# Optimization experiments

Measured on AMD Instinct MI355X. Metric: run time of the kernel, lower is better.

The kernel has to match this reference:

```python
import jax, jax.numpy as jnp
import numpy as np

EMB_SIZE = 768
BLOCK_SIZE = 64
OFFSET = 1  # bert cls offset


def setup_inputs() -> dict:
    key = jax.random.key(0)
    ks = jax.random.split(key, 10)
    n, c, d, h, E, M, P = 4, 1024, 768, 12, 42, 8, 1024
    sequence_output = jax.random.normal(ks[0], (n, c, d), jnp.float32)
    attention = jax.random.uniform(ks[1], (n, h, c, c), jnp.float32)
    attention = attention / attention.sum(-1, keepdims=True)  # softmax-like rows
    Wh = jax.random.normal(ks[2], (EMB_SIZE, 2 * d), jnp.float32) * 0.02
    bh = jax.random.normal(ks[3], (EMB_SIZE,), jnp.float32) * 0.02
    Wt = jax.random.normal(ks[4], (EMB_SIZE, 2 * d), jnp.float32) * 0.02
    bt = jax.random.normal(ks[5], (EMB_SIZE,), jnp.float32) * 0.02
    Wb = jax.random.normal(ks[6], (99, EMB_SIZE * BLOCK_SIZE), jnp.float32) * 0.02
    mention_pos = jax.random.randint(ks[7], (n, E, M), 0, c - 1 - OFFSET, jnp.int32)
    mention_mask = jax.random.randint(ks[8], (n, E, M), 0, 2, jnp.int32)
    mention_mask = mention_mask.at[:, :, 0].set(1)  # every entity has >=1 mention
    hts = jax.random.randint(ks[9], (n, P, 2), 0, E, jnp.int32)
    return {"sequence_output": sequence_output, "attention": attention,
            "Wh": Wh, "bh": bh, "Wt": Wt, "bt": bt, "Wb": Wb,
            "mention_pos": mention_pos, "mention_mask": mention_mask, "hts": hts}


def _get_hrt_doc(seq, att, pos, mask, ht):
    # seq [c,d], att [h,c,c], pos/mask [E,M], ht [P,2]
    p = pos + OFFSET                                   # [E,M]
    valid = mask > 0
    memb = seq[p]                                      # [E,M,d] gather
    e_emb = jax.scipy.special.logsumexp(
        jnp.where(valid[..., None], memb, -jnp.inf), axis=1)  # [E,d]
    matt = att[:, p]                                   # [h,E,M,c] gather
    cnt = valid.sum(1).astype(seq.dtype)               # [E]
    e_att = (matt * valid[None, :, :, None].astype(seq.dtype)).sum(2)
    e_att = jnp.transpose(e_att, (1, 0, 2)) / cnt[:, None, None]  # [E,h,c] mention mean
    hs = e_emb[ht[:, 0]]                               # [P,d]
    ts = e_emb[ht[:, 1]]
    h_att = e_att[ht[:, 0]]                            # [P,h,c]
    t_att = e_att[ht[:, 1]]
    ht_att = (h_att * t_att).mean(1)                   # [P,c] head mean
    ht_att = ht_att / (ht_att.sum(1, keepdims=True) + 1e-5)
    rs = jnp.einsum('ld,rl->rd', seq, ht_att)          # [P,d]
    return hs, ts, rs


def reference(sequence_output, attention, Wh, bh, Wt, bt, Wb,
              mention_pos, mention_mask, hts):
    d = sequence_output.shape[-1]
    hs, ts, rs = jax.vmap(_get_hrt_doc)(sequence_output, attention,
                                        mention_pos, mention_mask, hts)
    hs = hs.reshape(-1, d)
    ts = ts.reshape(-1, d)
    rs = rs.reshape(-1, d)
    hs = jnp.tanh(jnp.concatenate([hs, rs], axis=1) @ Wh.T + bh)
    ts = jnp.tanh(jnp.concatenate([ts, rs], axis=1) @ Wt.T + bt)
    nb = EMB_SIZE // BLOCK_SIZE
    b1 = hs.reshape(-1, nb, BLOCK_SIZE)
    b2 = ts.reshape(-1, nb, BLOCK_SIZE)
    bl = (b1[:, :, :, None] * b2[:, :, None, :]).reshape(-1, EMB_SIZE * BLOCK_SIZE)
    logits = bl @ Wb.T                                 # [N, num_labels+2]
    return logits
```

## Files before the change

### kernel.cpp

```cpp
#include <hip/hip_runtime.h>
#include <hip/hip_bf16.h>
#include <hip/hip_fp16.h>
#include <math.h>

#define NDOC 4
#define CCC  1024
#define DDD  768
#define HHH  12
#define EEE  42
#define MMM  8
#define PPP  1024
#define NBQ  12
#define NK   99
#define NPAD 112

typedef __attribute__((ext_vector_type(8))) short short8v;
typedef __attribute__((ext_vector_type(8))) _Float16 half8;
typedef __attribute__((ext_vector_type(4))) float floatx4;

__device__ __forceinline__ unsigned short f32_to_bf16u(float f) {
  return __builtin_bit_cast(unsigned short, __float2bfloat16(f));
}
__device__ __forceinline__ unsigned short f32_to_f16u(float f) {
  return __builtin_bit_cast(unsigned short, __float2half(f));
}

__global__ __launch_bounds__(256) void k_eemb(const float* __restrict__ seq,
    const int* __restrict__ pos, const int* __restrict__ mask,
    unsigned short* __restrict__ eembB) {
  int e = blockIdx.x, doc = blockIdx.y;
  int base = (doc*EEE + e)*MMM;
  int p[MMM], mk[MMM];
#pragma unroll
  for (int m = 0; m < MMM; ++m) { p[m] = pos[base+m] + 1; mk[m] = mask[base+m]; }
  for (int d0 = threadIdx.x; d0 < DDD; d0 += 256) {
    float v[MMM]; float mx = -INFINITY;
#pragma unroll
    for (int m = 0; m < MMM; ++m) {
      v[m] = seq[(doc*CCC + p[m])*DDD + d0];
      if (mk[m]) mx = fmaxf(mx, v[m]);
    }
    float s = 0.f;
#pragma unroll
    for (int m = 0; m < MMM; ++m) if (mk[m]) s += expf(v[m]-mx);
    eembB[(doc*EEE + e)*DDD + d0] = f32_to_bf16u(logf(s) + mx);
  }
}

__global__ __launch_bounds__(256) void k_eatt(const float* __restrict__ att,
    const int* __restrict__ pos, const int* __restrict__ mask,
    float* __restrict__ eatt) {
  int head = blockIdx.x, e = blockIdx.y, doc = blockIdx.z;
  int base = (doc*EEE + e)*MMM;
  int j = threadIdx.x * 4;
  float ax=0.f, ay=0.f, az=0.f, aw=0.f; float cnt = 0.f;
#pragma unroll
  for (int m = 0; m < MMM; ++m) {
    int mk = mask[base+m];
    cnt += (float)mk;
    if (mk) {
      int pp = pos[base+m] + 1;
      const float4 a = *(const float4*)&att[((size_t)(doc*HHH + head)*CCC + pp)*CCC + j];
      ax += a.x; ay += a.y; az += a.z; aw += a.w;
    }
  }
  float inv = 1.f / cnt;
  float4 o; o.x = ax*inv; o.y = ay*inv; o.z = az*inv; o.w = aw*inv;
  *(float4*)&eatt[((size_t)((doc*EEE + e)*HHH + head))*CCC + j] = o;
}

__global__ __launch_bounds__(256) void k_htatt(const float* __restrict__ eatt,
    const int* __restrict__ hts, unsigned short* __restrict__ htB) {
  int b = blockIdx.x; int doc = b >> 10; int r = b & 1023;
  int h0 = hts[(doc*PPP + r)*2 + 0];
  int t0 = hts[(doc*PPP + r)*2 + 1];
  const float* ea0 = &eatt[(size_t)((doc*EEE + h0)*HHH)*CCC];
  const float* ea1 = &eatt[(size_t)((doc*EEE + t0)*HHH)*CCC];
  int j = threadIdx.x * 4;
  float vx=0.f, vy=0.f, vz=0.f, vw=0.f;
#pragma unroll
  for (int hh = 0; hh < HHH; ++hh) {
    const float4 a  = *(const float4*)&ea0[hh*CCC + j];
    const float4 bq = *(const float4*)&ea1[hh*CCC + j];
    vx += a.x*bq.x; vy += a.y*bq.y; vz += a.z*bq.z; vw += a.w*bq.w;
  }
  const float inv12 = 1.f/12.f;
  vx *= inv12; vy *= inv12; vz *= inv12; vw *= inv12;
  float part = vx + vy + vz + vw;
  __shared__ float red[4];
  for (int off = 32; off > 0; off >>= 1) part += __shfl_down(part, off, 64);
  int lane = threadIdx.x & 63, wv = threadIdx.x >> 6;
  if (lane == 0) red[wv] = part;
  __syncthreads();
  if (threadIdx.x == 0) red[0] = red[0]+red[1]+red[2]+red[3];
  __syncthreads();
  float sc = 1.f / (red[0] + 1e-5f);
  unsigned short o[4];
  o[0] = f32_to_bf16u(vx*sc); o[1] = f32_to_bf16u(vy*sc);
  o[2] = f32_to_bf16u(vz*sc); o[3] = f32_to_bf16u(vw*sc);
  *(uint2*)&htB[((size_t)(doc*PPP + r))*CCC + j] = *(const uint2*)o;
}

__global__ __launch_bounds__(256) void k_packW(const float* __restrict__ Wh,
    const float* __restrict__ Wt, unsigned short* __restrict__ WB) {
  int gid = blockIdx.x*256 + threadIdx.x;
  int half = gid >= 147456;
  int loc = half ? gid - 147456 : gid;
  const float* src = (half ? Wt : Wh) + (size_t)loc*8;
  float4 v0 = *(const float4*)src;
  float4 v1 = *(const float4*)(src+4);
  unsigned short o[8];
  o[0]=f32_to_bf16u(v0.x); o[1]=f32_to_bf16u(v0.y); o[2]=f32_to_bf16u(v0.z); o[3]=f32_to_bf16u(v0.w);
  o[4]=f32_to_bf16u(v1.x); o[5]=f32_to_bf16u(v1.y); o[6]=f32_to_bf16u(v1.z); o[7]=f32_to_bf16u(v1.w);
  *(uint4*)&WB[(size_t)half*1179648 + (size_t)loc*8] = *(const uint4*)o;
}

__global__ __launch_bounds__(256) void k_seqT(const float* __restrict__ seq,
    unsigned short* __restrict__ seqTB) {
  __shared__ float tl[64][65];
  int d0 = blockIdx.x * 64, c0 = blockIdx.y * 64, doc = blockIdx.z;
  int t = threadIdx.x;
#pragma unroll
  for (int rep = 0; rep < 4; ++rep) {
    int cr = rep*16 + (t >> 4);
    int d4 = (t & 15) * 4;
    float4 v = *(const float4*)&seq[((size_t)doc*CCC + c0 + cr)*DDD + d0 + d4];
    tl[cr][d4+0]=v.x; tl[cr][d4+1]=v.y; tl[cr][d4+2]=v.z; tl[cr][d4+3]=v.w;
  }
  __syncthreads();
#pragma unroll
  for (int rep = 0; rep < 4; ++rep) {
    int dr = rep*16 + (t >> 4);
    int c4 = (t & 15) * 4;
    unsigned short o[4];
#pragma unroll
    for (int kq = 0; kq < 4; ++kq)
      o[kq] = f32_to_bf16u(tl[c4+kq][dr]);
    *(uint2*)&seqTB[((size_t)doc*DDD + d0 + dr)*CCC + c0 + c4] = *(const uint2*)o;
  }
}

__global__ __launch_bounds__(256) void k_rs_mfma(
    const unsigned short* __restrict__ htB,
    const unsigned short* __restrict__ seqTB,
    unsigned short* __restrict__ rsB) {
  __shared__ unsigned short A_l[4096];
  __shared__ unsigned short B_l[4096];
  const int n0 = blockIdx.x * 128;
  const int m0 = blockIdx.y * 128;
  const int doc = m0 >> 10;
  const int mloc = m0 & 1023;
  const int t = threadIdx.x;
  const int lane = t & 63;
  const int ln = lane & 15, q4 = lane >> 4;
  const int w = t >> 6;
  const int wr = w >> 1, wc = w & 1;

  const int r0 = t >> 2;
  const int koff = (t & 3) * 8;
  const unsigned short* srcA0 = htB + ((size_t)doc*CCC + mloc + r0)*CCC + koff;
  const unsigned short* srcA1 = htB + ((size_t)doc*CCC + mloc + r0 + 64)*CCC + koff;
  const unsigned short* srcB0 = seqTB + ((size_t)doc*DDD + n0 + r0)*CCC + koff;
  const unsigned short* srcB1 = seqTB + ((size_t)doc*DDD + n0 + r0 + 64)*CCC + koff;

  floatx4 acc[4][4];
#pragma unroll
  for (int i = 0; i < 4; ++i)
#pragma unroll
    for (int j = 0; j < 4; ++j) acc[i][j] = (floatx4){0.f,0.f,0.f,0.f};

  for (int k0 = 0; k0 < CCC; k0 += 32) {
    uint4 va0 = *(const uint4*)(srcA0 + k0);
    uint4 va1 = *(const uint4*)(srcA1 + k0);
    uint4 vb0 = *(const uint4*)(srcB0 + k0);
    uint4 vb1 = *(const uint4*)(srcB1 + k0);
    __syncthreads();
    *(uint4*)&A_l[(size_t)t*8]       = va0;
    *(uint4*)&A_l[(size_t)(t+256)*8] = va1;
    *(uint4*)&B_l[(size_t)t*8]       = vb0;
    *(uint4*)&B_l[(size_t)(t+256)*8] = vb1;
    __syncthreads();
    short8v a[4], b[4];
#pragma unroll
    for (int rt = 0; rt < 4; ++rt)
      a[rt] = *(const short8v*)&A_l[((wr*64 + rt*16 + ln)*4 + q4)*8];
#pragma unroll
    for (int nt = 0; nt < 4; ++nt)
      b[nt] = *(const short8v*)&B_l[((wc*64 + nt*16 + ln)*4 + q4)*8];
#pragma unroll
    for (int rt = 0; rt < 4; ++rt)
#pragma unroll
      for (int nt = 0; nt < 4; ++nt)
        acc[rt][nt] = __builtin_amdgcn_mfma_f32_16x16x32_bf16(a[rt], b[nt], acc[rt][nt], 0, 0, 0);
  }
#pragma unroll
  for (int rt = 0; rt < 4; ++rt)
#pragma unroll
    for (int nt = 0; nt < 4; ++nt) {
      int col = n0 + wc*64 + nt*16 + ln;
#pragma unroll
      for (int reg = 0; reg < 4; ++reg) {
        int row = m0 + wr*64 + rt*16 + q4*4 + reg;
        rsB[(size_t)row*DDD + col] = f32_to_bf16u(acc[rt][nt][reg]);
      }
    }
}

__global__ __launch_bounds__(256) void k_heads_mfma(
    const unsigned short* __restrict__ eembB,
    const unsigned short* __restrict__ rsB,
    const int* __restrict__ hts,
    const unsigned short* __restrict__ WB,
    const float* __restrict__ bh, const float* __restrict__ bt,
    float* __restrict__ hsb, float* __restrict__ tsb) {
  __shared__ unsigned short A_l[4096];
  __shared__ unsigned short B_l[4096];
  const int which = blockIdx.z;
  const int n0 = blockIdx.x * 128;
  const int m0 = blockIdx.y * 128;
  const int doc = m0 >> 10;
  const int t = threadIdx.x;
  const int lane = t & 63;
  const int ln = lane & 15, q4 = lane >> 4;
  const int w = t >> 6;
  const int wr = w >> 1, wc = w & 1;

  const int r0 = t >> 2;
  const int koff = (t & 3) * 8;
  const int rgA0 = m0 + r0, rgA1 = m0 + r0 + 64;
  const int idx0 = hts[rgA0*2 + which];
  const int idx1 = hts[rgA1*2 + which];
  const unsigned short* srcE0 = eembB + (size_t)(doc*EEE + idx0)*DDD + koff;
  const unsigned short* srcE1 = eembB + (size_t)(doc*EEE + idx1)*DDD + koff;
  const unsigned short* srcR0 = rsB + (size_t)rgA0*DDD + koff;
  const unsigned short* srcR1 = rsB + (size_t)rgA1*DDD + koff;
  const unsigned short* WBz = WB + (size_t)which*1179648;
  const unsigned short* srcW0 = WBz + (size_t)(n0 + r0)*1536 + koff;
  const unsigned short* srcW1 = WBz + (size_t)(n0 + r0 + 64)*1536 + koff;

  floatx4 acc[4][4];
#pragma unroll
  for (int i = 0; i < 4; ++i)
#pragma unroll
    for (int j = 0; j < 4; ++j) acc[i][j] = (floatx4){0.f,0.f,0.f,0.f};

  for (int k0 = 0; k0 < 1536; k0 += 32) {
    uint4 va0 = (k0 < DDD) ? *(const uint4*)(srcE0 + k0) : *(const uint4*)(srcR0 + (k0 - DDD));
    uint4 va1 = (k0 < DDD) ? *(const uint4*)(srcE1 + k0) : *(const uint4*)(srcR1 + (k0 - DDD));
    uint4 vb0 = *(const uint4*)(srcW0 + k0);
    uint4 vb1 = *(const uint4*)(srcW1 + k0);
    __syncthreads();
    *(uint4*)&A_l[(size_t)t*8]       = va0;
    *(uint4*)&A_l[(size_t)(t+256)*8] = va1;
    *(uint4*)&B_l[(size_t)t*8]       = vb0;
    *(uint4*)&B_l[(size_t)(t+256)*8] = vb1;
    __syncthreads();
    short8v a[4], b[4];
#pragma unroll
    for (int rt = 0; rt < 4; ++rt)
      a[rt] = *(const short8v*)&A_l[((wr*64 + rt*16 + ln)*4 + q4)*8];
#pragma unroll
    for (int nt = 0; nt < 4; ++nt)
      b[nt] = *(const short8v*)&B_l[((wc*64 + nt*16 + ln)*4 + q4)*8];
#pragma unroll
    for (int rt = 0; rt < 4; ++rt)
#pragma unroll
      for (int nt = 0; nt < 4; ++nt)
        acc[rt][nt] = __builtin_amdgcn_mfma_f32_16x16x32_bf16(a[rt], b[nt], acc[rt][nt], 0, 0, 0);
  }
  const float* bias = which ? bt : bh;
  float* outp = which ? tsb : hsb;
#pragma unroll
  for (int rt = 0; rt < 4; ++rt)
#pragma unroll
    for (int nt = 0; nt < 4; ++nt) {
      int col = n0 + wc*64 + nt*16 + ln;
      float bsv = bias[col];
#pragma unroll
      for (int reg = 0; reg < 4; ++reg) {
        int row = m0 + wr*64 + rt*16 + q4*4 + reg;
        outp[(size_t)row*DDD + col] = tanhf(acc[rt][nt][reg] + bsv);
      }
    }
}

__global__ __launch_bounds__(256) void k_prep_w(const float* __restrict__ Wb,
    unsigned short* __restrict__ Wp) {
  int t = blockIdx.x*256 + threadIdx.x;
  int j8 = (t & 7) * 8;
  int n = (t >> 3) % NPAD;
  int ki = t / 896;
  unsigned short o[8];
  if (n < NK) {
    const float* src = &Wb[(size_t)n*49152 + ki*64 + j8];
    float4 v0 = *(const float4*)src;
    float4 v1 = *(const float4*)(src+4);
    o[0]=f32_to_f16u(v0.x); o[1]=f32_to_f16u(v0.y); o[2]=f32_to_f16u(v0.z); o[3]=f32_to_f16u(v0.w);
    o[4]=f32_to_f16u(v1.x); o[5]=f32_to_f16u(v1.y); o[6]=f32_to_f16u(v1.z); o[7]=f32_to_f16u(v1.w);
  } else {
#pragma unroll
    for (int e=0;e<8;++e) o[e]=0;
  }
  int js = (t & 7) >> 2, q = t & 3;
  int nt = n >> 4, lnn = n & 15;
  int c = ((js*7 + nt)*4 + q)*16 + lnn;
  *(uint4*)&Wp[(size_t)ki*7168 + c*8] = *(const uint4*)o;
}

__global__ __launch_bounds__(256) void k_pack_hs(const float* __restrict__ hs,
    unsigned short* __restrict__ hsT) {
  __shared__ float tl[64][65];
  int i0 = blockIdx.x * 64, r0 = blockIdx.y * 64;
  int t = threadIdx.x;
#pragma unroll
  for (int rep = 0; rep < 4; ++rep) {
    int r = rep*16 + (t >> 4);
    int c4 = (t & 15) * 4;
    float4 v = *(const float4*)&hs[(size_t)(r0 + r)*DDD + i0 + c4];
    tl[r][c4+0]=v.x; tl[r][c4+1]=v.y; tl[r][c4+2]=v.z; tl[r][c4+3]=v.w;
  }
  __syncthreads();
#pragma unroll
  for (int rep = 0; rep < 4; ++rep) {
    int i = rep*16 + (t >> 4);
    int r4 = (t & 15) * 4;
    unsigned short o[4];
#pragma unroll
    for (int kq = 0; kq < 4; ++kq)
      o[kq] = f32_to_f16u(tl[r4+kq][i]);
    *(uint2*)&hsT[(size_t)(i0 + i)*4096 + r0 + r4] = *(const uint2*)o;
  }
}

__global__ __launch_bounds__(128, 2) void k_logits_mfma(
    const unsigned short* __restrict__ hsT,
    const float* __restrict__ tsb,
    const unsigned short* __restrict__ Wp,
    unsigned short* __restrict__ P) {
  __shared__ unsigned short hsT_l[32*128];
  __shared__ unsigned short Bt_l[2*7168];
  const int slice = blockIdx.x;
  const int kbase = (slice >> 1)*64 + (slice & 1)*32;
  const int mtile = blockIdx.y;
  const int t = threadIdx.x;
  const int w = t >> 6;
  const int lane = t & 63;
  const int ln = lane & 15;
  const int q = lane >> 4;
  const int m0w = mtile*128 + w*64;

#pragma unroll
  for (int rep = 0; rep < 4; ++rep) {
    int c16 = t + rep*128;
    int ii = c16 >> 4;
    int c8 = (c16 & 15) * 8;
    uint4 v = *(const uint4*)&hsT[(size_t)(kbase + ii)*4096 + mtile*128 + c8];
    *(uint4*)&hsT_l[ii*128 + c8] = v;
  }

  __half2 tsr2[4][2][4];
  {
    int nb = kbase >> 6;
#pragma unroll
    for (int rt = 0; rt < 4; ++rt) {
      int row = m0w + rt*16 + ln;
#pragma unroll
      for (int js = 0; js < 2; ++js) {
        const float* p = &tsb[(size_t)row*DDD + nb*64 + js*32 + q*8];
        float4 v0 = *(const float4*)p;
        float4 v1 = *(const float4*)(p+4);
        tsr2[rt][js][0] = __floats2half2_rn(v0.x, v0.y);
        tsr2[rt][js][1] = __floats2half2_rn(v0.z, v0.w);
        tsr2[rt][js][2] = __floats2half2_rn(v1.x, v1.y);
        tsr2[rt][js][3] = __floats2half2_rn(v1.z, v1.w);
      }
    }
  }

  floatx4 acc[4][7];
#pragma unroll
  for (int rt = 0; rt < 4; ++rt)
#pragma unroll
    for (int nt = 0; nt < 7; ++nt)
      acc[rt][nt] = (floatx4){0.f,0.f,0.f,0.f};

  uint4 wreg[7];
#pragma unroll
  for (int r = 0; r < 7; ++r)
    wreg[r] = *(const uint4*)&Wp[(size_t)kbase*7168 + (t + r*128)*8];
#pragma unroll
  for (int r = 0; r < 7; ++r)
    *(uint4*)&Bt_l[(t + r*128)*8] = wreg[r];
  __syncthreads();

  for (int ii = 0; ii < 32; ++ii) {
    const unsigned short* bufc = Bt_l + (ii & 1)*7168;
    if (ii < 31) {
      int ki = kbase + ii + 1;
#pragma unroll
      for (int r = 0; r < 7; ++r)
        wreg[r] = *(const uint4*)&Wp[(size_t)ki*7168 + (t + r*128)*8];
    }
    __half2 hh[4];
#pragma unroll
    for (int rt = 0; rt < 4; ++rt) {
      unsigned short hb = hsT_l[ii*128 + w*64 + rt*16 + ln];
      hh[rt] = __half2half2(__ushort_as_half(hb));
    }
#pragma unroll
    for (int js = 0; js < 2; ++js) {
      half8 a[4];
#pragma unroll
      for (int rt = 0; rt < 4; ++rt) {
        uint4 au;
        au.x = __builtin_bit_cast(unsigned int, __hmul2(hh[rt], tsr2[rt][js][0]));
        au.y = __builtin_bit_cast(unsigned int, __hmul2(hh[rt], tsr2[rt][js][1]));
        au.z = __builtin_bit_cast(unsigned int, __hmul2(hh[rt], tsr2[rt][js][2]));
        au.w = __builtin_bit_cast(unsigned int, __hmul2(hh[rt], tsr2[rt][js][3]));
        a[rt] = __builtin_bit_cast(half8, au);
      }
#pragma unroll
      for (int nt = 0; nt < 7; ++nt) {
        half8 b = __builtin_bit_cast(half8,
            *(const short8v*)&bufc[((js*7 + nt)*4)*128 + lane*8]);
#pragma unroll
        for (int rt = 0; rt < 4; ++rt)
          acc[rt][nt] = __builtin_amdgcn_mfma_f32_16x16x32_f16(a[rt], b, acc[rt][nt], 0, 0, 0);
      }
    }
    if (ii < 31) {
      __syncthreads();
#pragma unroll
      for (int r = 0; r < 7; ++r)
        *(uint4*)&Bt_l[((ii+1) & 1)*7168 + (t + r*128)*8] = wreg[r];
      __syncthreads();
    }
  }

  unsigned short* Ps = P + (size_t)slice*(4096*NPAD);
#pragma unroll
  for (int nt = 0; nt < 7; ++nt) {
    int col = nt*16 + ln;
#pragma unroll
    for (int rt = 0; rt < 4; ++rt) {
#pragma unroll
      for (int reg = 0; reg < 4; ++reg) {
        int row = m0w + rt*16 + q*4 + reg;
        Ps[(size_t)row*NPAD + col] = f32_to_f16u(acc[rt][nt][reg]);
      }
    }
  }
}

__global__ __launch_bounds__(256) void k_logred(const unsigned short* __restrict__ P,
    float* __restrict__ out) {
  int idx = blockIdx.x*256 + threadIdx.x;
  int r = idx / NPAD;
  int c = idx % NPAD;
  if (c >= NK) return;
  float s = 0.f;
#pragma unroll
  for (int sl = 0; sl < 24; ++sl)
    s += __half2float(__ushort_as_half(P[(size_t)sl*(4096*NPAD) + idx]));
  out[(size_t)r*NK + c] = s;
}

extern "C" void kernel_launch(void* const* d_in, const int* in_sizes, int n_in,
                              void* d_out, int out_size, void* d_ws, size_t ws_size,
                              hipStream_t stream) {
  const float* seq  = (const float*)d_in[0];
  const float* att  = (const float*)d_in[1];
  const float* Wh   = (const float*)d_in[2];
  const float* bh   = (const float*)d_in[3];
  const float* Wt   = (const float*)d_in[4];
  const float* bt   = (const float*)d_in[5];
  const float* Wb   = (const float*)d_in[6];
  const int* pos    = (const int*)d_in[7];
  const int* mask   = (const int*)d_in[8];
  const int* hts    = (const int*)d_in[9];
  float* out = (float*)d_out;

  float* ws = (float*)d_ws;
  float*          eatt  = ws;
  unsigned short* htB   = (unsigned short*)(ws + 2064384);
  unsigned short* eembB = (unsigned short*)(ws + 4161536);
  unsigned short* seqTB = (unsigned short*)(ws + 4226048);
  unsigned short* WhtB  = (unsigned short*)(ws + 5798912);
  unsigned short* rsB   = (unsigned short*)(ws + 6978560);
  float*          hsb   = ws + 8551424;
  float*          tsb   = ws + 11697152;
  unsigned short* WpB   = (unsigned short*)eatt;
  unsigned short* hsTB  = (unsigned short*)seqTB;
  unsigned short* Pp    = (unsigned short*)(ws + 5798912);

  k_eemb<<<dim3(EEE, NDOC), 256, 0, stream>>>(seq, pos, mask, eembB);
  k_eatt<<<dim3(HHH, EEE, NDOC), 256, 0, stream>>>(att, pos, mask, eatt);
  k_htatt<<<dim3(NDOC*PPP), 256, 0, stream>>>(eatt, hts, htB);
  k_packW<<<dim3(1152), 256, 0, stream>>>(Wh, Wt, WhtB);
  k_seqT<<<dim3(DDD/64, CCC/64, NDOC), 256, 0, stream>>>(seq, seqTB);
  k_rs_mfma<<<dim3(6, 32), 256, 0, stream>>>(htB, seqTB, rsB);
  k_prep_w<<<dim3(2688), 256, 0, stream>>>(Wb, WpB);
  k_heads_mfma<<<dim3(6, 32, 2), 256, 0, stream>>>(eembB, rsB, hts, WhtB, bh, bt, hsb, tsb);
  k_pack_hs<<<dim3(DDD/64, 4096/64), 256, 0, stream>>>(hsb, hsTB);
  k_logits_mfma<<<dim3(24, 32), 128, 0, stream>>>(hsTB, tsb, WpB, Pp);
  k_logred<<<dim3(4096*NPAD/256), 256, 0, stream>>>(Pp, out);
}
```

Measured before the change: 221.8 us.

## Merge prep kernels, restructure ht-attention via LDS tiles, emit fp16 heads directly

Five independent preprocessing kernels (entity embedding, entity attention, Wh/Wt pack, seq transpose, Wb pack) become one block-dispatched kernel, cutting launch overhead and serialization. The per-pair ht-attention kernel is split into a tiled pass that caches per-entity attention in LDS and writes partial sums, followed by a normalization pass. The heads GEMM now writes fp16 transposed hs through LDS and fp16 ts directly, which removes the separate pack_hs kernel and the fp32 intermediates. Costs are a larger workspace, an extra 16 MB unnormalized fp32 buffer, and more LDS per heads block, which may reduce occupancy.

```diff
diff --git a/kernel.cpp b/kernel.cpp
--- a/kernel.cpp
+++ b/kernel.cpp
@@ -10,9 +10,9 @@
 #define EEE  42
 #define MMM  8
 #define PPP  1024
-#define NBQ  12
 #define NK   99
 #define NPAD 112
+#define NSLICE 24
 
 typedef __attribute__((ext_vector_type(8))) short short8v;
 typedef __attribute__((ext_vector_type(8))) _Float16 half8;
@@ -25,119 +25,163 @@
   return __builtin_bit_cast(unsigned short, __float2half(f));
 }
 
-__global__ __launch_bounds__(256) void k_eemb(const float* __restrict__ seq,
+__global__ __launch_bounds__(256) void k_prep(
+    const float* __restrict__ seq, const float* __restrict__ att,
+    const float* __restrict__ Wh, const float* __restrict__ Wt,
+    const float* __restrict__ Wb,
     const int* __restrict__ pos, const int* __restrict__ mask,
-    unsigned short* __restrict__ eembB) {
-  int e = blockIdx.x, doc = blockIdx.y;
-  int base = (doc*EEE + e)*MMM;
-  int p[MMM], mk[MMM];
-#pragma unroll
-  for (int m = 0; m < MMM; ++m) { p[m] = pos[base+m] + 1; mk[m] = mask[base+m]; }
-  for (int d0 = threadIdx.x; d0 < DDD; d0 += 256) {
-    float v[MMM]; float mx = -INFINITY;
+    unsigned short* __restrict__ eembB, float* __restrict__ eatt,
+    unsigned short* __restrict__ WhtB, unsigned short* __restrict__ seqTB,
+    unsigned short* __restrict__ WpB) {
+  const int bx = blockIdx.x;
+  const int tid = threadIdx.x;
+  if (bx < 168) {
+    int e = bx % EEE, doc = bx / EEE;
+    int base = (doc*EEE + e)*MMM;
+    int p[MMM], mk[MMM];
+#pragma unroll
+    for (int m = 0; m < MMM; ++m) { p[m] = pos[base+m] + 1; mk[m] = mask[base+m]; }
+    for (int d0 = tid; d0 < DDD; d0 += 256) {
+      float v[MMM]; float mx = -INFINITY;
+#pragma unroll
+      for (int m = 0; m < MMM; ++m) {
+        v[m] = seq[(doc*CCC + p[m])*DDD + d0];
+        if (mk[m]) mx = fmaxf(mx, v[m]);
+      }
+      float s = 0.f;
+#pragma unroll
+      for (int m = 0; m < MMM; ++m) if (mk[m]) s += expf(v[m]-mx);
+      eembB[(doc*EEE + e)*DDD + d0] = f32_to_bf16u(logf(s) + mx);
+    }
+  } else if (bx < 2184) {
+    int b = bx - 168;
+    int head = b % HHH, e = (b/HHH) % EEE, doc = b / (HHH*EEE);
+    int base = (doc*EEE + e)*MMM;
+    int j = tid * 4;
+    float ax=0.f, ay=0.f, az=0.f, aw=0.f; float cnt = 0.f;
 #pragma unroll
     for (int m = 0; m < MMM; ++m) {
-      v[m] = seq[(doc*CCC + p[m])*DDD + d0];
-      if (mk[m]) mx = fmaxf(mx, v[m]);
-    }
-    float s = 0.f;
-#pragma unroll
-    for (int m = 0; m < MMM; ++m) if (mk[m]) s += expf(v[m]-mx);
-    eembB[(doc*EEE + e)*DDD + d0] = f32_to_bf16u(logf(s) + mx);
-  }
-}
-
-__global__ __launch_bounds__(256) void k_eatt(const float* __restrict__ att,
-    const int* __restrict__ pos, const int* __restrict__ mask,
-    float* __restrict__ eatt) {
-  int head = blockIdx.x, e = blockIdx.y, doc = blockIdx.z;
-  int base = (doc*EEE + e)*MMM;
-  int j = threadIdx.x * 4;
-  float ax=0.f, ay=0.f, az=0.f, aw=0.f; float cnt = 0.f;
-#pragma unroll
-  for (int m = 0; m < MMM; ++m) {
-    int mk = mask[base+m];
-    cnt += (float)mk;
-    if (mk) {
-      int pp = pos[base+m] + 1;
-      const float4 a = *(const float4*)&att[((size_t)(doc*HHH + head)*CCC + pp)*CCC + j];
-      ax += a.x; ay += a.y; az += a.z; aw += a.w;
-    }
-  }
-  float inv = 1.f / cnt;
-  float4 o; o.x = ax*inv; o.y = ay*inv; o.z = az*inv; o.w = aw*inv;
-  *(float4*)&eatt[((size_t)((doc*EEE + e)*HHH + head))*CCC + j] = o;
-}
-
-__global__ __launch_bounds__(256) void k_htatt(const float* __restrict__ eatt,
-    const int* __restrict__ hts, unsigned short* __restrict__ htB) {
-  int b = blockIdx.x; int doc = b >> 10; int r = b & 1023;
-  int h0 = hts[(doc*PPP + r)*2 + 0];
-  int t0 = hts[(doc*PPP + r)*2 + 1];
-  const float* ea0 = &eatt[(size_t)((doc*EEE + h0)*HHH)*CCC];
-  const float* ea1 = &eatt[(size_t)((doc*EEE + t0)*HHH)*CCC];
-  int j = threadIdx.x * 4;
-  float vx=0.f, vy=0.f, vz=0.f, vw=0.f;
-#pragma unroll
-  for (int hh = 0; hh < HHH; ++hh) {
-    const float4 a  = *(const float4*)&ea0[hh*CCC + j];
-    const float4 bq = *(const float4*)&ea1[hh*CCC + j];
-    vx += a.x*bq.x; vy += a.y*bq.y; vz += a.z*bq.z; vw += a.w*bq.w;
-  }
-  const float inv12 = 1.f/12.f;
-  vx *= inv12; vy *= inv12; vz *= inv12; vw *= inv12;
-  float part = vx + vy + vz + vw;
-  __shared__ float red[4];
-  for (int off = 32; off > 0; off >>= 1) part += __shfl_down(part, off, 64);
-  int lane = threadIdx.x & 63, wv = threadIdx.x >> 6;
-  if (lane == 0) red[wv] = part;
+      int mk = mask[base+m];
+      cnt += (float)mk;
+      if (mk) {
+        int pp = pos[base+m] + 1;
+        const float4 a = *(const float4*)&att[((size_t)(doc*HHH + head)*CCC + pp)*CCC + j];
+        ax += a.x; ay += a.y; az += a.z; aw += a.w;
+      }
+    }
+    float inv = 1.f / cnt;
+    float4 o; o.x = ax*inv; o.y = ay*inv; o.z = az*inv; o.w = aw*inv;
+    *(float4*)&eatt[((size_t)((doc*EEE + e)*HHH + head))*CCC + j] = o;
+  } else if (bx < 3336) {
+    int gid = (bx - 2184)*256 + tid;
+    int half = gid >= 147456;
+    int loc = half ? gid - 147456 : gid;
+    const float* src = (half ? Wt : Wh) + (size_t)loc*8;
+    float4 v0 = *(const float4*)src;
+    float4 v1 = *(const float4*)(src+4);
+    unsigned short o[8];
+    o[0]=f32_to_bf16u(v0.x); o[1]=f32_to_bf16u(v0.y); o[2]=f32_to_bf16u(v0.z); o[3]=f32_to_bf16u(v0.w);
+    o[4]=f32_to_bf16u(v1.x); o[5]=f32_to_bf16u(v1.y); o[6]=f32_to_bf16u(v1.z); o[7]=f32_to_bf16u(v1.w);
+    *(uint4*)&WhtB[(size_t)half*1179648 + (size_t)loc*8] = *(const uint4*)o;
+  } else if (bx < 4104) {
+    __shared__ float tl[64][65];
+    int b = bx - 3336;
+    int d0 = (b % 12)*64, c0 = ((b/12) % 16)*64, doc = b / 192;
+#pragma unroll
+    for (int rep = 0; rep < 4; ++rep) {
+      int cr = rep*16 + (tid >> 4);
+      int d4 = (tid & 15) * 4;
+      float4 v = *(const float4*)&seq[((size_t)doc*CCC + c0 + cr)*DDD + d0 + d4];
+      tl[cr][d4+0]=v.x; tl[cr][d4+1]=v.y; tl[cr][d4+2]=v.z; tl[cr][d4+3]=v.w;
+    }
+    __syncthreads();
+#pragma unroll
+    for (int rep = 0; rep < 4; ++rep) {
+      int dr = rep*16 + (tid >> 4);
+      int c4 = (tid & 15) * 4;
+      unsigned short o[4];
+#pragma unroll
+      for (int kq = 0; kq < 4; ++kq)
+        o[kq] = f32_to_bf16u(tl[c4+kq][dr]);
+      *(uint2*)&seqTB[((size_t)doc*DDD + d0 + dr)*CCC + c0 + c4] = *(const uint2*)o;
+    }
+  } else {
+    int t = (bx - 4104)*256 + tid;
+    int j8 = (t & 7) * 8;
+    int n = (t >> 3) % NPAD;
+    int ki = t / 896;
+    unsigned short o[8];
+    if (n < NK) {
+      const float* src = &Wb[(size_t)n*49152 + ki*64 + j8];
+      float4 v0 = *(const float4*)src;
+      float4 v1 = *(const float4*)(src+4);
+      o[0]=f32_to_f16u(v0.x); o[1]=f32_to_f16u(v0.y); o[2]=f32_to_f16u(v0.z); o[3]=f32_to_f16u(v0.w);
+      o[4]=f32_to_f16u(v1.x); o[5]=f32_to_f16u(v1.y); o[6]=f32_to_f16u(v1.z); o[7]=f32_to_f16u(v1.w);
+    } else {
+#pragma unroll
+      for (int e=0;e<8;++e) o[e]=0;
+    }
+    int js = (t & 7) >> 2, q = t & 3;
+    int nt = n >> 4, lnn = n & 15;
+    int c = ((js*7 + nt)*4 + q)*16 + lnn;
+    *(uint4*)&WpB[(size_t)ki*7168 + c*8] = *(const uint4*)o;
+  }
+}
+
+__global__ __launch_bounds__(256) void k_htatt1(const float* __restrict__ eatt,
+    const int* __restrict__ hts, float* __restrict__ htU,
+    float* __restrict__ Ssum) {
+  __shared__ float tile[EEE*16*12];
+  const int cg = blockIdx.x, doc = blockIdx.y;
+  const int c0 = cg * 16;
+  for (int idx = threadIdx.x; idx < EEE*16*12; idx += 256) {
+    int e = idx / 192, rem = idx % 192, h = rem / 16, cc = rem % 16;
+    tile[(e*16 + cc)*12 + h] =
+        eatt[((size_t)((doc*EEE + e)*HHH + h))*CCC + c0 + cc];
+  }
   __syncthreads();
-  if (threadIdx.x == 0) red[0] = red[0]+red[1]+red[2]+red[3];
+  const int cc = threadIdx.x & 15;
+  const int pg = threadIdx.x >> 4;
+  for (int it = 0; it < 64; ++it) {
+    int p = pg + it*16;
+    int h0 = hts[(doc*PPP + p)*2 + 0];
+    int t0 = hts[(doc*PPP + p)*2 + 1];
+    const float* a = &tile[(h0*16 + cc)*12];
+    const float* b = &tile[(t0*16 + cc)*12];
+    float4 a0 = *(const float4*)a,     b0 = *(const float4*)b;
+    float4 a1 = *(const float4*)(a+4), b1 = *(const float4*)(b+4);
+    float4 a2 = *(const float4*)(a+8), b2 = *(const float4*)(b+8);
+    float s = a0.x*b0.x + a0.y*b0.y + a0.z*b0.z + a0.w*b0.w
+            + a1.x*b1.x + a1.y*b1.y + a1.z*b1.z + a1.w*b1.w
+            + a2.x*b2.x + a2.y*b2.y + a2.z*b2.z + a2.w*b2.w;
+    s *= (1.f/12.f);
+    htU[((size_t)(doc*PPP + p))*CCC + c0 + cc] = s;
+    float r = s;
+    r += __shfl_xor(r, 1, 16);
+    r += __shfl_xor(r, 2, 16);
+    r += __shfl_xor(r, 4, 16);
+    r += __shfl_xor(r, 8, 16);
+    if (cc == 0) Ssum[((size_t)(doc*PPP + p))*64 + cg] = r;
+  }
+}
+
+__global__ __launch_bounds__(256) void k_htnorm(const float* __restrict__ htU,
+    const float* __restrict__ Ssum, unsigned short* __restrict__ htB) {
+  __shared__ float sc_sh;
+  const int b = blockIdx.x;
+  const int lane = threadIdx.x;
+  if (lane < 64) {
+    float r = Ssum[(size_t)b*64 + lane];
+    for (int off = 32; off > 0; off >>= 1) r += __shfl_down(r, off, 64);
+    if (lane == 0) sc_sh = 1.f / (r + 1e-5f);
+  }
   __syncthreads();
-  float sc = 1.f / (red[0] + 1e-5f);
+  float sc = sc_sh;
+  float4 v = *(const float4*)&htU[(size_t)b*CCC + lane*4];
   unsigned short o[4];
-  o[0] = f32_to_bf16u(vx*sc); o[1] = f32_to_bf16u(vy*sc);
-  o[2] = f32_to_bf16u(vz*sc); o[3] = f32_to_bf16u(vw*sc);
-  *(uint2*)&htB[((size_t)(doc*PPP + r))*CCC + j] = *(const uint2*)o;
-}
-
-__global__ __launch_bounds__(256) void k_packW(const float* __restrict__ Wh,
-    const float* __restrict__ Wt, unsigned short* __restrict__ WB) {
-  int gid = blockIdx.x*256 + threadIdx.x;
-  int half = gid >= 147456;
-  int loc = half ? gid - 147456 : gid;
-  const float* src = (half ? Wt : Wh) + (size_t)loc*8;
-  float4 v0 = *(const float4*)src;
-  float4 v1 = *(const float4*)(src+4);
-  unsigned short o[8];
-  o[0]=f32_to_bf16u(v0.x); o[1]=f32_to_bf16u(v0.y); o[2]=f32_to_bf16u(v0.z); o[3]=f32_to_bf16u(v0.w);
-  o[4]=f32_to_bf16u(v1.x); o[5]=f32_to_bf16u(v1.y); o[6]=f32_to_bf16u(v1.z); o[7]=f32_to_bf16u(v1.w);
-  *(uint4*)&WB[(size_t)half*1179648 + (size_t)loc*8] = *(const uint4*)o;
-}
-
-__global__ __launch_bounds__(256) void k_seqT(const float* __restrict__ seq,
-    unsigned short* __restrict__ seqTB) {
-  __shared__ float tl[64][65];
-  int d0 = blockIdx.x * 64, c0 = blockIdx.y * 64, doc = blockIdx.z;
-  int t = threadIdx.x;
-#pragma unroll
-  for (int rep = 0; rep < 4; ++rep) {
-    int cr = rep*16 + (t >> 4);
-    int d4 = (t & 15) * 4;
-    float4 v = *(const float4*)&seq[((size_t)doc*CCC + c0 + cr)*DDD + d0 + d4];
-    tl[cr][d4+0]=v.x; tl[cr][d4+1]=v.y; tl[cr][d4+2]=v.z; tl[cr][d4+3]=v.w;
-  }
-  __syncthreads();
-#pragma unroll
-  for (int rep = 0; rep < 4; ++rep) {
-    int dr = rep*16 + (t >> 4);
-    int c4 = (t & 15) * 4;
-    unsigned short o[4];
-#pragma unroll
-    for (int kq = 0; kq < 4; ++kq)
-      o[kq] = f32_to_bf16u(tl[c4+kq][dr]);
-    *(uint2*)&seqTB[((size_t)doc*DDD + d0 + dr)*CCC + c0 + c4] = *(const uint2*)o;
-  }
+  o[0] = f32_to_bf16u(v.x*sc); o[1] = f32_to_bf16u(v.y*sc);
+  o[2] = f32_to_bf16u(v.z*sc); o[3] = f32_to_bf16u(v.w*sc);
+  *(uint2*)&htB[(size_t)b*CCC + lane*4] = *(const uint2*)o;
 }
 
 __global__ __launch_bounds__(256) void k_rs_mfma(
@@ -212,9 +256,11 @@
     const int* __restrict__ hts,
     const unsigned short* __restrict__ WB,
     const float* __restrict__ bh, const float* __restrict__ bt,
-    float* __restrict__ hsb, float* __restrict__ tsb) {
+    unsigned short* __restrict__ hsTB,
+    unsigned short* __restrict__ tsbH) {
   __shared__ unsigned short A_l[4096];
   __shared__ unsigned short B_l[4096];
+  __shared__ unsigned short T_l[128*144];
   const int which = blockIdx.z;
   const int n0 = blockIdx.x * 128;
   const int m0 = blockIdx.y * 128;
@@ -269,78 +315,53 @@
         acc[rt][nt] = __builtin_amdgcn_mfma_f32_16x16x32_bf16(a[rt], b[nt], acc[rt][nt], 0, 0, 0);
   }
   const float* bias = which ? bt : bh;
-  float* outp = which ? tsb : hsb;
-#pragma unroll
-  for (int rt = 0; rt < 4; ++rt)
-#pragma unroll
-    for (int nt = 0; nt < 4; ++nt) {
-      int col = n0 + wc*64 + nt*16 + ln;
-      float bsv = bias[col];
-#pragma unroll
-      for (int reg = 0; reg < 4; ++reg) {
-        int row = m0 + wr*64 + rt*16 + q4*4 + reg;
-        outp[(size_t)row*DDD + col] = tanhf(acc[rt][nt][reg] + bsv);
-      }
-    }
-}
-
-__global__ __launch_bounds__(256) void k_prep_w(const float* __restrict__ Wb,
-    unsigned short* __restrict__ Wp) {
-  int t = blockIdx.x*256 + threadIdx.x;
-  int j8 = (t & 7) * 8;
-  int n = (t >> 3) % NPAD;
-  int ki = t / 896;
-  unsigned short o[8];
-  if (n < NK) {
-    const float* src = &Wb[(size_t)n*49152 + ki*64 + j8];
-    float4 v0 = *(const float4*)src;
-    float4 v1 = *(const float4*)(src+4);
-    o[0]=f32_to_f16u(v0.x); o[1]=f32_to_f16u(v0.y); o[2]=f32_to_f16u(v0.z); o[3]=f32_to_f16u(v0.w);
-    o[4]=f32_to_f16u(v1.x); o[5]=f32_to_f16u(v1.y); o[6]=f32_to_f16u(v1.z); o[7]=f32_to_f16u(v1.w);
+  if (which == 0) {
+#pragma unroll
+    for (int rt = 0; rt < 4; ++rt)
+#pragma unroll
+      for (int nt = 0; nt < 4; ++nt) {
+        int col = wc*64 + nt*16 + ln;
+        float bsv = bias[n0 + col];
+#pragma unroll
+        for (int reg = 0; reg < 4; ++reg) {
+          int row = wr*64 + rt*16 + q4*4 + reg;
+          T_l[col*144 + row] = f32_to_f16u(tanhf(acc[rt][nt][reg] + bsv));
+        }
+      }
+    __syncthreads();
+#pragma unroll
+    for (int iter = 0; iter < 8; ++iter) {
+      int col = iter*16 + (t >> 4);
+      int rblk = t & 15;
+      uint4 v = *(const uint4*)&T_l[col*144 + rblk*8];
+      *(uint4*)&hsTB[(size_t)(n0 + col)*4096 + m0 + rblk*8] = v;
+    }
   } else {
 #pragma unroll
-    for (int e=0;e<8;++e) o[e]=0;
-  }
-  int js = (t & 7) >> 2, q = t & 3;
-  int nt = n >> 4, lnn = n & 15;
-  int c = ((js*7 + nt)*4 + q)*16 + lnn;
-  *(uint4*)&Wp[(size_t)ki*7168 + c*8] = *(const uint4*)o;
-}
-
-__global__ __launch_bounds__(256) void k_pack_hs(const float* __restrict__ hs,
-    unsigned short* __restrict__ hsT) {
-  __shared__ float tl[64][65];
-  int i0 = blockIdx.x * 64, r0 = blockIdx.y * 64;
-  int t = threadIdx.x;
-#pragma unroll
-  for (int rep = 0; rep < 4; ++rep) {
-    int r = rep*16 + (t >> 4);
-    int c4 = (t & 15) * 4;
-    float4 v = *(const float4*)&hs[(size_t)(r0 + r)*DDD + i0 + c4];
-    tl[r][c4+0]=v.x; tl[r][c4+1]=v.y; tl[r][c4+2]=v.z; tl[r][c4+3]=v.w;
-  }
-  __syncthreads();
-#pragma unroll
-  for (int rep = 0; rep < 4; ++rep) {
-    int i = rep*16 + (t >> 4);
-    int r4 = (t & 15) * 4;
-    unsigned short o[4];
-#pragma unroll
-    for (int kq = 0; kq < 4; ++kq)
-      o[kq] = f32_to_f16u(tl[r4+kq][i]);
-    *(uint2*)&hsT[(size_t)(i0 + i)*4096 + r0 + r4] = *(const uint2*)o;
-  }
-}
-
-__global__ __launch_bounds__(128, 2) void k_logits_mfma(
+    for (int rt = 0; rt < 4; ++rt)
+#pragma unroll
+      for (int nt = 0; nt < 4; ++nt) {
+        int col = n0 + wc*64 + nt*16 + ln;
+        float bsv = bias[col];
+#pragma unroll
+        for (int reg = 0; reg < 4; ++reg) {
+          int row = m0 + wr*64 + rt*16 + q4*4 + reg;
+          tsbH[(size_t)row*DDD + col] = f32_to_f16u(tanhf(acc[rt][nt][reg] + bsv));
+        }
+      }
+  }
+}
+
+__global__ __launch_bounds__(128) void k_logits_mfma(
     const unsigned short* __restrict__ hsT,
-    const float* __restrict__ tsb,
+    const unsigned short* __restrict__ tsbH,
     const unsigned short* __restrict__ Wp,
     unsigned short* __restrict__ P) {
   __shared__ unsigned short hsT_l[32*128];
   __shared__ unsigned short Bt_l[2*7168];
   const int slice = blockIdx.x;
   const int kbase = (slice >> 1)*64 + (slice & 1)*32;
+  const int nb = slice >> 1;
   const int mtile = blockIdx.y;
   const int t = threadIdx.x;
   const int w = t >> 6;
@@ -359,21 +380,16 @@
   }
 
   __half2 tsr2[4][2][4];
-  {
-    int nb = kbase >> 6;
-#pragma unroll
-    for (int rt = 0; rt < 4; ++rt) {
-      int row = m0w + rt*16 + ln;
-#pragma unroll
-      for (int js = 0; js < 2; ++js) {
-        const float* p = &tsb[(size_t)row*DDD + nb*64 + js*32 + q*8];
-        float4 v0 = *(const float4*)p;
-        float4 v1 = *(const float4*)(p+4);
-        tsr2[rt][js][0] = __floats2half2_rn(v0.x, v0.y);
-        tsr2[rt][js][1] = __floats2half2_rn(v0.z, v0.w);
-        tsr2[rt][js][2] = __floats2half2_rn(v1.x, v1.y);
-        tsr2[rt][js][3] = __floats2half2_rn(v1.z, v1.w);
-      }
+#pragma unroll
+  for (int rt = 0; rt < 4; ++rt) {
+    int row = m0w + rt*16 + ln;
+#pragma unroll
+    for (int js = 0; js < 2; ++js) {
+      uint4 v = *(const uint4*)&tsbH[(size_t)row*DDD + nb*64 + js*32 + q*8];
+      tsr2[rt][js][0] = __builtin_bit_cast(__half2, v.x);
+      tsr2[rt][js][1] = __builtin_bit_cast(__half2, v.y);
+      tsr2[rt][js][2] = __builtin_bit_cast(__half2, v.z);
+      tsr2[rt][js][3] = __builtin_bit_cast(__half2, v.w);
     }
   }
 
@@ -460,7 +476,7 @@
   if (c >= NK) return;
   float s = 0.f;
 #pragma unroll
-  for (int sl = 0; sl < 24; ++sl)
+  for (int sl = 0; sl < NSLICE; ++sl)
     s += __half2float(__ushort_as_half(P[(size_t)sl*(4096*NPAD) + idx]));
   out[(size_t)r*NK + c] = s;
 }
@@ -482,26 +498,24 @@
 
   float* ws = (float*)d_ws;
   float*          eatt  = ws;
-  unsigned short* htB   = (unsigned short*)(ws + 2064384);
-  unsigned short* eembB = (unsigned short*)(ws + 4161536);
-  unsigned short* seqTB = (unsigned short*)(ws + 4226048);
-  unsigned short* WhtB  = (unsigned short*)(ws + 5798912);
-  unsigned short* rsB   = (unsigned short*)(ws + 6978560);
-  float*          hsb   = ws + 8551424;
-  float*          tsb   = ws + 11697152;
-  unsigned short* WpB   = (unsigned short*)eatt;
-  unsigned short* hsTB  = (unsigned short*)seqTB;
-  unsigned short* Pp    = (unsigned short*)(ws + 5798912);
-
-  k_eemb<<<dim3(EEE, NDOC), 256, 0, stream>>>(seq, pos, mask, eembB);
-  k_eatt<<<dim3(HHH, EEE, NDOC), 256, 0, stream>>>(att, pos, mask, eatt);
-  k_htatt<<<dim3(NDOC*PPP), 256, 0, stream>>>(eatt, hts, htB);
-  k_packW<<<dim3(1152), 256, 0, stream>>>(Wh, Wt, WhtB);
-  k_seqT<<<dim3(DDD/64, CCC/64, NDOC), 256, 0, stream>>>(seq, seqTB);
+  float*          htU   = ws + 2064384;
+  float*          Ssum  = ws + 6258688;
+  unsigned short* htB   = (unsigned short*)(ws + 6520832);
+  unsigned short* eembB = (unsigned short*)(ws + 8617984);
+  unsigned short* seqTB = (unsigned short*)(ws + 8682496);
+  unsigned short* WhtB  = (unsigned short*)(ws + 10255360);
+  unsigned short* rsB   = (unsigned short*)(ws + 11435008);
+  unsigned short* hsTB  = (unsigned short*)(ws + 13007872);
+  unsigned short* tsbH  = (unsigned short*)(ws + 14580736);
+  unsigned short* WpB   = (unsigned short*)(ws + 16153600);
+  unsigned short* Pp    = (unsigned short*)(ws + 18906112);
+
+  k_prep<<<dim3(6792), 256, 0, stream>>>(seq, att, Wh, Wt, Wb, pos, mask,
+                                         eembB, eatt, WhtB, seqTB, WpB);
+  k_htatt1<<<dim3(64, NDOC), 256, 0, stream>>>(eatt, hts, htU, Ssum);
+  k_htnorm<<<dim3(NDOC*PPP), 256, 0, stream>>>(htU, Ssum, htB);
   k_rs_mfma<<<dim3(6, 32), 256, 0, stream>>>(htB, seqTB, rsB);
-  k_prep_w<<<dim3(2688), 256, 0, stream>>>(Wb, WpB);
-  k_heads_mfma<<<dim3(6, 32, 2), 256, 0, stream>>>(eembB, rsB, hts, WhtB, bh, bt, hsb, tsb);
-  k_pack_hs<<<dim3(DDD/64, 4096/64), 256, 0, stream>>>(hsb, hsTB);
-  k_logits_mfma<<<dim3(24, 32), 128, 0, stream>>>(hsTB, tsb, WpB, Pp);
+  k_heads_mfma<<<dim3(6, 32, 2), 256, 0, stream>>>(eembB, rsB, hts, WhtB, bh, bt, hsTB, tsbH);
+  k_logits_mfma<<<dim3(NSLICE, 32), 128, 0, stream>>>(hsTB, tsbH, WpB, Pp);
   k_logred<<<dim3(4096*NPAD/256), 256, 0, stream>>>(Pp, out);
 }
```

After: 264.7 us. 1.19x slower.
